# Performance work log

Measured on AMD Instinct MI355X. Metric: run time of the kernel, lower is better.

Reference implementation:

```python
import jax, jax.numpy as jnp
import numpy as np

NUM_HEADS = 128
QK_NOPE = 128
QK_ROPE = 64
V_HEAD = 128
Q_HEAD_DIM = 192
SOFTMAX_SCALE = 1.0 / np.sqrt(192.0)


def _rope_interleave(x, cos, sin):
    # x: [b,h,s,d]; reorder interleaved pairs to half-split layout then rotate
    b, h, s, d = x.shape
    x = x.reshape(b, h, s, d // 2, 2).swapaxes(3, 4).reshape(b, h, s, d)
    x1, x2 = x[..., : d // 2], x[..., d // 2:]
    rot = jnp.concatenate([-x2, x1], axis=-1)
    return x * cos + rot * sin


def setup_inputs() -> dict:
    key = jax.random.key(0)
    ks = jax.random.split(key, 8)
    bsz, q_len = 16, 1
    q_lora, kv_lora = 1536, 512
    cache_cap = 4096
    start_pos = 2048
    s = 0.05
    q_normed_dn = jax.random.normal(ks[0], (bsz, q_len, q_lora), jnp.float32) * s
    compressed_kv = jax.random.normal(ks[1], (bsz, q_len, kv_lora), jnp.float32) * s
    k_pe = jax.random.normal(ks[2], (bsz, 1, q_len, QK_ROPE), jnp.float32) * s
    position_ids = jnp.full((bsz, q_len), start_pos, dtype=jnp.int64)
    ckv_cache = jax.random.normal(ks[3], (bsz, cache_cap, kv_lora), jnp.float32) * s
    k_pe_cache = jax.random.normal(ks[4], (bsz, cache_cap, QK_ROPE), jnp.float32) * s
    # rope caches over full positions
    pos = jnp.arange(cache_cap, dtype=jnp.float32)
    inv = 1.0 / (10000.0 ** (jnp.arange(0, QK_ROPE, 2, dtype=jnp.float32) / QK_ROPE))
    freqs = pos[:, None] * inv[None, :]
    emb = jnp.concatenate([freqs, freqs], axis=-1)
    sin_cache = jnp.sin(emb)
    cos_cache = jnp.cos(emb)
    wkv_b = jax.random.normal(ks[5], (NUM_HEADS, QK_NOPE + V_HEAD, kv_lora), jnp.float32) * s
    wq_b = jax.random.normal(ks[6], (NUM_HEADS * Q_HEAD_DIM, q_lora), jnp.float32) * s
    return {
        "q_normed_dn": q_normed_dn,
        "compressed_kv": compressed_kv,
        "k_pe": k_pe,
        "position_ids": position_ids,
        "start_pos": start_pos,
        "ckv_cache": ckv_cache,
        "k_pe_cache": k_pe_cache,
        "sin_cache": sin_cache,
        "cos_cache": cos_cache,
        "wkv_b": wkv_b,
        "wq_b": wq_b,
    }


def reference(q_normed_dn, compressed_kv, k_pe, position_ids, start_pos,
              ckv_cache, k_pe_cache, sin_cache, cos_cache, wkv_b, wq_b):
    bsz, q_len, q_lora = q_normed_dn.shape
    kv_lora = compressed_kv.shape[-1]

    # split absorbed query projection
    wq_b_t = wq_b.T.reshape(q_lora, NUM_HEADS, Q_HEAD_DIM)  # [l,h,192]
    q_nope = jnp.einsum('bsl,lhd->bhsd', q_normed_dn, wq_b_t[:, :, :QK_NOPE])
    q_pe = jnp.einsum('bsl,lhd->bhsd', q_normed_dn, wq_b_t[:, :, QK_NOPE:])

    # matrix absorption: q_nope projected into latent space via w_ukv
    w_ukv = wkv_b[:, :QK_NOPE]                         # [h,128,c]
    q_nope = jnp.einsum('bshd,hdc->bshc', q_nope.swapaxes(1, 2), w_ukv)  # [b,s,h,c]

    # RoPE on q_pe and k_pe using gathered cos/sin at position_ids
    cos = cos_cache[position_ids][:, None]   # [b,1,s,d]
    sin = sin_cache[position_ids][:, None]
    q_pe = _rope_interleave(q_pe, cos, sin)            # [b,h,s,64]
    k_pe = _rope_interleave(k_pe, cos, sin)            # [b,1,s,64]
    q_pe = q_pe.swapaxes(1, 2)                         # [b,s,h,64]
    k_pe = k_pe[:, 0]                                  # [b,s,64]

    # append new tokens to caches at start_pos (q_len new tokens)
    ckv_cache = jax.lax.dynamic_update_slice(ckv_cache, compressed_kv, (0, start_pos, 0))
    k_pe_cache = jax.lax.dynamic_update_slice(k_pe_cache, k_pe, (0, start_pos, 0))
    kv_len = start_pos + q_len
    ckv = ckv_cache[:, :kv_len]                        # [b,n,c]
    kpe = k_pe_cache[:, :kv_len]                       # [b,n,64]

    # MLA decode attention in latent space (q_len==1, causal trivially satisfied)
    # scores = q_nope . ckv + q_pe . kpe
    scores = (jnp.einsum('bshc,bnc->bhsn', q_nope, ckv) +
              jnp.einsum('bshd,bnd->bhsn', q_pe, kpe)) * SOFTMAX_SCALE
    probs = jax.nn.softmax(scores, axis=-1)
    o = jnp.einsum('bhsn,bnc->bshc', probs, ckv)       # [b,s,h,c]
    o = o.reshape(bsz * q_len, NUM_HEADS, kv_lora)

    # project latent output to v_head_dim via tail of wkv_b
    attn_output = jnp.einsum('bhc,hdc->bhd', o, wkv_b[:, -V_HEAD:])
    return attn_output
```

## Files before the change

kernel.cpp:

```cpp
#include <hip/hip_runtime.h>
#include <hip/hip_bf16.h>
#include <math.h>

typedef __attribute__((ext_vector_type(8))) short short8x;
typedef __attribute__((ext_vector_type(4))) float f32x4;
typedef __attribute__((ext_vector_type(4))) unsigned short u16x4;
typedef __attribute__((ext_vector_type(8))) unsigned short u16x8;

#define NSPLIT 16
#define NTILE 66
#define KVROWS (NTILE * 32)

__device__ __forceinline__ unsigned short f2bf(float x) {
  unsigned int u = __float_as_uint(x);
  u += 0x7fffu + ((u >> 16) & 1u);
  return (unsigned short)(u >> 16);
}
__device__ __forceinline__ float bf2f(unsigned short u) {
  return __uint_as_float(((unsigned int)u) << 16);
}
__device__ __forceinline__ u16x4 cvt4(float4 v) {
  u16x4 r;
  r[0] = f2bf(v.x); r[1] = f2bf(v.y); r[2] = f2bf(v.z); r[3] = f2bf(v.w);
  return r;
}
__device__ __forceinline__ void gload_lds16(const void* g, void* l) {
  __builtin_amdgcn_global_load_lds(
      (const __attribute__((address_space(1))) unsigned int*)g,
      (__attribute__((address_space(3))) unsigned int*)l, 16, 0, 0);
}

__global__ __launch_bounds__(256, 4) void kA(
    const float* __restrict__ ckvc, const float* __restrict__ kpec,
    const float* __restrict__ ckvn, const float* __restrict__ kpein,
    const float* __restrict__ cosc, const float* __restrict__ sinc,
    const int* __restrict__ sposp, int cap,
    unsigned short* __restrict__ kvbf,
    const float* __restrict__ wq, const float* __restrict__ x,
    float* __restrict__ qpart) {
  const int bx = blockIdx.x;
  const int tid = threadIdx.x;

  if (bx < 1536) {
    const int rowblock = bx >> 2, kq = bx & 3;
    const int lane = tid & 63, wid = tid >> 6;
    const int l15 = lane & 15, lg = lane >> 4;
    const int rowb = rowblock * 64 + wid * 16;
    const float* wrow = wq + (size_t)(rowb + l15) * 1536 + kq * 384 + lg * 8;
    const float* xrow = x + (size_t)l15 * 1536 + kq * 384 + lg * 8;

    f32x4 aHH = (f32x4){0.f, 0.f, 0.f, 0.f};
    f32x4 aHL = (f32x4){0.f, 0.f, 0.f, 0.f};
    f32x4 aLH = (f32x4){0.f, 0.f, 0.f, 0.f};
    f32x4 bHH = (f32x4){0.f, 0.f, 0.f, 0.f};
    f32x4 bHL = (f32x4){0.f, 0.f, 0.f, 0.f};
    f32x4 bLH = (f32x4){0.f, 0.f, 0.f, 0.f};

    float4 wA[2], wB[2], xA[2], xB[2];
#pragma unroll
    for (int i = 0; i < 2; ++i) {
      wA[i] = *(const float4*)(wrow + i * 32);
      wB[i] = *(const float4*)(wrow + i * 32 + 4);
      xA[i] = *(const float4*)(xrow + i * 32);
      xB[i] = *(const float4*)(xrow + i * 32 + 4);
    }

#pragma unroll
    for (int kc = 0; kc < 12; ++kc) {
      const int s = kc & 1;
      const float wf[8] = {wA[s].x, wA[s].y, wA[s].z, wA[s].w,
                           wB[s].x, wB[s].y, wB[s].z, wB[s].w};
      const float xf[8] = {xA[s].x, xA[s].y, xA[s].z, xA[s].w,
                           xB[s].x, xB[s].y, xB[s].z, xB[s].w};
      short8x ah, al, bh, bl;
#pragma unroll
      for (int e = 0; e < 8; ++e) {
        const unsigned int wu = __float_as_uint(wf[e]);
        const float whf = __uint_as_float(wu & 0xffff0000u);
        ah[e] = (short)(wu >> 16);
        al[e] = (short)(__float_as_uint(wf[e] - whf) >> 16);
        const unsigned int xu = __float_as_uint(xf[e]);
        const float xhf = __uint_as_float(xu & 0xffff0000u);
        bh[e] = (short)(xu >> 16);
        bl[e] = (short)(__float_as_uint(xf[e] - xhf) >> 16);
      }
      if (kc + 2 < 12) {
        wA[s] = *(const float4*)(wrow + (kc + 2) * 32);
        wB[s] = *(const float4*)(wrow + (kc + 2) * 32 + 4);
        xA[s] = *(const float4*)(xrow + (kc + 2) * 32);
        xB[s] = *(const float4*)(xrow + (kc + 2) * 32 + 4);
      }
      if (kc & 1) {
        bHH = __builtin_amdgcn_mfma_f32_16x16x32_bf16(ah, bh, bHH, 0, 0, 0);
        bHL = __builtin_amdgcn_mfma_f32_16x16x32_bf16(ah, bl, bHL, 0, 0, 0);
        bLH = __builtin_amdgcn_mfma_f32_16x16x32_bf16(al, bh, bLH, 0, 0, 0);
      } else {
        aHH = __builtin_amdgcn_mfma_f32_16x16x32_bf16(ah, bh, aHH, 0, 0, 0);
        aHL = __builtin_amdgcn_mfma_f32_16x16x32_bf16(ah, bl, aHL, 0, 0, 0);
        aLH = __builtin_amdgcn_mfma_f32_16x16x32_bf16(al, bh, aLH, 0, 0, 0);
      }
    }
    const f32x4 acc = (aHH + bHH) + (aHL + bHL) + (aLH + bLH);
#pragma unroll
    for (int r = 0; r < 4; ++r)
      qpart[(size_t)kq * 393216 + (size_t)l15 * 24576 + rowb + lg * 4 + r] = acc[r];
  } else {
    const int bxx = bx - 1536;
    const int spos = sposp[0];
    float4 va[4], vb[4];
    int nn[4], cc[4], bg[4];
#pragma unroll
    for (int g = 0; g < 4; ++g) {
      const int u = bxx * 1024 + g * 256 + tid;
      const int b = u / 152064;
      const int r = u - b * 152064;
      const int n = r / 72;
      const int c8 = (r - n * 72) * 8;
      bg[g] = b; nn[g] = n; cc[g] = c8;
      const float* s0;
      if (n < spos) {
        s0 = (c8 < 512) ? ckvc + ((size_t)b * cap + n) * 512 + c8
                        : kpec + ((size_t)b * cap + n) * 64 + (c8 - 512);
      } else if (n == spos && c8 < 512) {
        s0 = ckvn + (size_t)b * 512 + c8;
      } else {
        s0 = ckvc;
      }
      va[g] = *(const float4*)s0;
      vb[g] = *(const float4*)(s0 + 4);
    }
#pragma unroll
    for (int g = 0; g < 4; ++g) {
      const int u = bxx * 1024 + g * 256 + tid;
      const int n = nn[g], c8 = cc[g], b = bg[g];
      u16x8 w;
      if (n > spos) {
#pragma unroll
        for (int k = 0; k < 8; ++k) w[k] = 0;
      } else if (n == spos && c8 >= 512) {
        const int d = c8 - 512;
        const float* kp = kpein + b * 64;
#pragma unroll
        for (int k = 0; k < 8; ++k) {
          const int dd = d + k;
          const int j = (dd < 32) ? dd : dd - 32;
          const float cj = cosc[spos * 64 + j], sj = sinc[spos * 64 + j];
          const float val = (dd < 32) ? kp[2 * j] * cj - kp[2 * j + 1] * sj
                                      : kp[2 * j + 1] * cj + kp[2 * j] * sj;
          w[k] = f2bf(val);
        }
      } else {
        const u16x4 lo = cvt4(va[g]), hi = cvt4(vb[g]);
#pragma unroll
        for (int k = 0; k < 4; ++k) { w[k] = lo[k]; w[4 + k] = hi[k]; }
      }
      *(u16x8*)(kvbf + (size_t)u * 8) = w;
    }
  }
}

__global__ __launch_bounds__(256) void kB2(
    const float* __restrict__ qpart, const float* __restrict__ wkv,
    const float* __restrict__ cosc, const float* __restrict__ sinc,
    const int* __restrict__ sposp, unsigned short* __restrict__ qcat,
    const unsigned short* __restrict__ kvbf, unsigned short* __restrict__ vT) {
  __shared__ __align__(16) unsigned char shbuf[36864];
  const int bx = blockIdx.x;
  const int tid = threadIdx.x;

  if (bx < 256) {
    float* qs = (float*)shbuf;
    const int h = bx & 127;
    const int half = bx >> 7;
    for (int u = tid; u < 2048; u += 256) {
      int bb = u >> 7, d = u & 127;
      const size_t off = (size_t)bb * 24576 + h * 192 + d;
      qs[u] = qpart[off] + qpart[off + 393216] +
              qpart[off + 786432] + qpart[off + 1179648];
    }
    __syncthreads();
    const int c = half * 256 + tid;
    float acc[16];
#pragma unroll
    for (int bb = 0; bb < 16; ++bb) acc[bb] = 0.f;
    const float* wbase = wkv + (size_t)h * 256 * 512;
    for (int d = 0; d < 128; ++d) {
      const float w = wbase[d * 512 + c];
#pragma unroll
      for (int bb = 0; bb < 16; ++bb) acc[bb] += qs[bb * 128 + d] * w;
    }
#pragma unroll
    for (int bb = 0; bb < 16; ++bb)
      qcat[(size_t)(bb * 128 + h) * 576 + c] = f2bf(acc[bb]);
  } else if (bx < 272) {
    const int b = bx - 256;
    const int pos = sposp[0];
#pragma unroll
    for (int i = 0; i < 16; ++i) {
      int idx = tid + i * 256;
      int h = idx >> 5, j = idx & 31;
      const float cj = cosc[pos * 64 + j];
      const float sj = sinc[pos * 64 + j];
      const size_t base = (size_t)b * 24576 + h * 192 + 128;
      float x0 = qpart[base + 2 * j] + qpart[base + 2 * j + 393216] +
                 qpart[base + 2 * j + 786432] + qpart[base + 2 * j + 1179648];
      float x1 = qpart[base + 2 * j + 1] + qpart[base + 2 * j + 1 + 393216] +
                 qpart[base + 2 * j + 1 + 786432] + qpart[base + 2 * j + 1 + 1179648];
      unsigned short* dst = qcat + (size_t)(b * 128 + h) * 576 + 512;
      dst[j] = f2bf(x0 * cj - x1 * sj);
      dst[j + 32] = f2bf(x1 * cj + x0 * sj);
    }
  } else {
    unsigned short* tile_sh = (unsigned short*)shbuf;
    const int v_ = bx - 272;
    const int b = v_ / NTILE;
    const int tile = v_ - b * NTILE;
    const int wid = tid >> 6;
    const unsigned short* src = kvbf + ((size_t)b * KVROWS + tile * 32) * 576;
#pragma unroll
    for (int i = 0; i < 9; ++i) {
      const int ch = i * 256 + tid;
      const int row = ch / 72, cc = ch - row * 72;
      gload_lds16(src + row * 576 + ((cc ^ (row & 7)) * 8),
                  &tile_sh[(i * 256 + wid * 64) * 8]);
    }
    __syncthreads();
    unsigned short* vdst = vT + ((size_t)b * NTILE + tile) * 18432;
#pragma unroll
    for (int r = 0; r < 9; ++r) {
      const int c = r * 64 + (tid >> 2);
      const int q = tid & 3;
      const int c8 = c >> 3, c7 = c & 7;
      u16x8 w;
#pragma unroll
      for (int j = 0; j < 8; ++j)
        w[j] = tile_sh[(q * 8 + j) * 576 + ((c8 ^ j) << 3) + c7];
      *(u16x8*)(vdst + c * 32 + q * 8) = w;
    }
  }
}

__global__ __launch_bounds__(512, 2) void k4_attn(
    const unsigned short* __restrict__ kvbf, const unsigned short* __restrict__ vT,
    const unsigned short* __restrict__ qcat, const int* __restrict__ sposp,
    unsigned short* __restrict__ opart, float* __restrict__ mlp) {
  __shared__ __align__(16) unsigned short kv_sh[2][32 * 576];
  __shared__ __align__(16) unsigned short vt_sh[2][512 * 32];
  __shared__ __align__(16) unsigned short p_sh[8 * 640];

  const int tid = threadIdx.x;
  const int split = blockIdx.x, b = blockIdx.y;
  const int kvlen = sposp[0] + 1;
  const int lane = tid & 63, wid = tid >> 6;
  const int l15 = lane & 15, lg = lane >> 4;

  const unsigned short* kvb = kvbf + (size_t)b * KVROWS * 576;
  const unsigned short* vtb = vT + (size_t)b * NTILE * 18432;

  const int vro = lane >> 2, vq = lane & 3;
  const int vgq = vq ^ ((vro >> 1) & 3);

  auto STAGE = [&](int pb, int tt) {
    const unsigned short* ksrc = kvb + (size_t)tt * 32 * 576;
    for (int j = wid; j < 36; j += 8) {
      int u = j * 64 + lane;
      int row = u / 72, cc = u - row * 72;
      gload_lds16(ksrc + row * 576 + ((cc ^ (row & 7)) * 8), &kv_sh[pb][j * 512]);
    }
    const unsigned short* vsrc = vtb + (size_t)tt * 18432;
    for (int j = wid; j < 32; j += 8)
      gload_lds16(vsrc + j * 512 + vro * 32 + vgq * 8, &vt_sh[pb][j * 512]);
  };

  STAGE(0, split);

  const int hrow = b * 128 + wid * 16 + l15;
  const unsigned short* qrow = qcat + (size_t)hrow * 576;
  short8x qf[18];
#pragma unroll
  for (int s = 0; s < 18; ++s)
    qf[s] = *(const short8x*)(qrow + s * 32 + lg * 8);

  f32x4 acc[32];
#pragma unroll
  for (int i = 0; i < 32; ++i) acc[i] = (f32x4){0.f, 0.f, 0.f, 0.f};
  float mold[4] = {-1e30f, -1e30f, -1e30f, -1e30f};
  float lsum[4] = {0.f, 0.f, 0.f, 0.f};
  const float C2 = (1.0f / sqrtf(192.0f)) * 1.4426950408889634f;

  const int vrd = ((lg ^ ((l15 >> 1) & 3)) << 3);

  int pb = 0;
  for (int tt = split; tt * 32 < kvlen; tt += NSPLIT, pb ^= 1) {
    __syncthreads();
    if ((tt + NSPLIT) * 32 < kvlen) STAGE(pb ^ 1, tt + NSPLIT);
    const int n0 = tt * 32;

    f32x4 D0 = (f32x4){0.f, 0.f, 0.f, 0.f};
    f32x4 D1 = (f32x4){0.f, 0.f, 0.f, 0.f};
#pragma unroll
    for (int s = 0; s < 18; ++s) {
      const int c8 = (s * 4 + lg) ^ (l15 & 7);
      short8x fb0 = *(const short8x*)&kv_sh[pb][l15 * 576 + c8 * 8];
      short8x fb1 = *(const short8x*)&kv_sh[pb][(16 + l15) * 576 + c8 * 8];
      D0 = __builtin_amdgcn_mfma_f32_16x16x32_bf16(qf[s], fb0, D0, 0, 0, 0);
      D1 = __builtin_amdgcn_mfma_f32_16x16x32_bf16(qf[s], fb1, D1, 0, 0, 0);
    }

    const bool v0 = (n0 + l15) < kvlen;
    const bool v1 = (n0 + 16 + l15) < kvlen;
    float alpha[4];
#pragma unroll
    for (int r = 0; r < 4; ++r) {
      const float t0 = v0 ? D0[r] * C2 : -1e30f;
      const float t1 = v1 ? D1[r] * C2 : -1e30f;
      float mx = fmaxf(t0, t1);
      mx = fmaxf(mx, __shfl_xor(mx, 1, 64));
      mx = fmaxf(mx, __shfl_xor(mx, 2, 64));
      mx = fmaxf(mx, __shfl_xor(mx, 4, 64));
      mx = fmaxf(mx, __shfl_xor(mx, 8, 64));
      const float mn = fmaxf(mold[r], mx);
      alpha[r] = exp2f(mold[r] - mn);
      const float p0 = v0 ? exp2f(t0 - mn) : 0.f;
      const float p1 = v1 ? exp2f(t1 - mn) : 0.f;
      float rs = p0 + p1;
      rs += __shfl_xor(rs, 1, 64);
      rs += __shfl_xor(rs, 2, 64);
      rs += __shfl_xor(rs, 4, 64);
      rs += __shfl_xor(rs, 8, 64);
      lsum[r] = lsum[r] * alpha[r] + rs;
      mold[r] = mn;
      p_sh[wid * 640 + (lg * 4 + r) * 40 + l15] = f2bf(p0);
      p_sh[wid * 640 + (lg * 4 + r) * 40 + 16 + l15] = f2bf(p1);
    }
    const f32x4 av = {alpha[0], alpha[1], alpha[2], alpha[3]};
#pragma unroll
    for (int cg = 0; cg < 32; ++cg) acc[cg] *= av;

    const short8x pa = *(const short8x*)&p_sh[wid * 640 + l15 * 40 + lg * 8];
#pragma unroll
    for (int cg = 0; cg < 32; ++cg) {
      short8x bv = *(const short8x*)&vt_sh[pb][cg * 512 + l15 * 32 + vrd];
      acc[cg] = __builtin_amdgcn_mfma_f32_16x16x32_bf16(pa, bv, acc[cg], 0, 0, 0);
    }
  }

  const int hbm_ = b * 128 + wid * 16 + lg * 4;
  if (l15 == 0) {
#pragma unroll
    for (int r = 0; r < 4; ++r) {
      mlp[(size_t)(hbm_ + r) * (2 * NSPLIT) + split * 2] = mold[r];
      mlp[(size_t)(hbm_ + r) * (2 * NSPLIT) + split * 2 + 1] = lsum[r];
    }
  }

  __syncthreads();
  unsigned short* ep = &kv_sh[0][0] + wid * 8192;
#pragma unroll
  for (int cg = 0; cg < 32; ++cg)
#pragma unroll
    for (int r = 0; r < 4; ++r)
      ep[(lg * 4 + r) * 512 + cg * 16 + l15] = f2bf(acc[cg][r]);
#pragma unroll
  for (int r16 = 0; r16 < 16; ++r16) {
    const int bh = b * 128 + wid * 16 + r16;
    const size_t ob = ((size_t)bh * NSPLIT + split) * 512;
#pragma unroll
    for (int i = 0; i < 2; ++i)
      *(u16x4*)&opart[ob + i * 256 + lane * 4] =
          *(const u16x4*)&ep[r16 * 512 + i * 256 + lane * 4];
  }
}

__global__ __launch_bounds__(512) void kC_out(
    const unsigned short* __restrict__ opart, const float* __restrict__ mlp,
    const float* __restrict__ wkv, float* __restrict__ out) {
  __shared__ float os[16 * 512];
  __shared__ float wsc[16 * 16];
  __shared__ float lsc[16];
  const int h = blockIdx.x;
  const int tid = threadIdx.x;

  if (tid < 16) {
    const int b = tid;
    const float* m = mlp + (size_t)(b * 128 + h) * (2 * NSPLIT);
    float mi[NSPLIT], li[NSPLIT], M = -1e30f;
#pragma unroll
    for (int i = 0; i < NSPLIT; ++i) {
      mi[i] = m[i * 2];
      li[i] = m[i * 2 + 1];
      M = fmaxf(M, mi[i]);
    }
    float Ls = 0.f;
#pragma unroll
    for (int i = 0; i < NSPLIT; ++i) {
      const float w = exp2f(mi[i] - M);
      Ls += li[i] * w;
      wsc[b * NSPLIT + i] = w;
    }
    lsc[b] = Ls;
  }
  __syncthreads();

  for (int u = tid; u < 8192; u += 512) {
    const int b = u >> 9, c = u & 511;
    const unsigned short* op = opart + (size_t)(b * 128 + h) * NSPLIT * 512 + c;
    float o = 0.f;
#pragma unroll
    for (int i = 0; i < NSPLIT; ++i) o += wsc[b * NSPLIT + i] * bf2f(op[i * 512]);
    os[u] = o / lsc[b];
  }
  __syncthreads();

  const int d = tid >> 2, cq = tid & 3;
  const float* wrow = wkv + ((size_t)(h * 256 + 128 + d)) * 512;
  float acc[16];
#pragma unroll
  for (int bb = 0; bb < 16; ++bb) acc[bb] = 0.f;
  for (int i = 0; i < 32; ++i) {
    const int c = cq * 4 + i * 16;
    const float4 w4 = *(const float4*)&wrow[c];
#pragma unroll
    for (int bb = 0; bb < 16; ++bb) {
      const float4 o4 = *(const float4*)&os[bb * 512 + c];
      acc[bb] += w4.x * o4.x + w4.y * o4.y + w4.z * o4.z + w4.w * o4.w;
    }
  }
#pragma unroll
  for (int bb = 0; bb < 16; ++bb) {
    float v = acc[bb];
    v += __shfl_xor(v, 1, 64);
    v += __shfl_xor(v, 2, 64);
    if (cq == 0) out[(size_t)(bb * 128 + h) * 128 + d] = v;
  }
}

extern "C" void kernel_launch(void* const* d_in, const int* in_sizes, int n_in,
                              void* d_out, int out_size, void* d_ws, size_t ws_size,
                              hipStream_t stream) {
  const float* x = (const float*)d_in[0];
  const float* ckvn = (const float*)d_in[1];
  const float* kpein = (const float*)d_in[2];
  const int* sposp = (const int*)d_in[4];
  const float* ckvc = (const float*)d_in[5];
  const float* kpec = (const float*)d_in[6];
  const float* sinc = (const float*)d_in[7];
  const float* cosc = (const float*)d_in[8];
  const float* wkv = (const float*)d_in[9];
  const float* wq = (const float*)d_in[10];
  float* out = (float*)d_out;

  const int cap = in_sizes[5] / (16 * 512);

  float* ws = (float*)d_ws;
  float* qpart = ws;
  float* mlp = ws + 1572864;
  unsigned short* qcat = (unsigned short*)(ws + 1638400);
  unsigned short* kvbf = (unsigned short*)(ws + 2228224);
  unsigned short* vT   = (unsigned short*)(ws + 11960320);
  unsigned short* opart = (unsigned short*)(ws + 21692416);

  kA<<<dim3(1536 + 2376), 256, 0, stream>>>(ckvc, kpec, ckvn, kpein, cosc, sinc,
                                            sposp, cap, kvbf, wq, x, qpart);
  kB2<<<dim3(272 + NTILE * 16), 256, 0, stream>>>(qpart, wkv, cosc, sinc, sposp,
                                                  qcat, kvbf, vT);
  k4_attn<<<dim3(NSPLIT, 16), 512, 0, stream>>>(kvbf, vT, qcat, sposp, opart, mlp);
  kC_out<<<dim3(128), 512, 0, stream>>>(opart, mlp, wkv, out);
}
```

Baseline: 164.3 us.

## Stage KV cache conversion through LDS with async global-to-LDS loads per tile

The fp32-to-bf16 KV cache conversion path in kA now gives each block a 16-row tile of one batch. Full tiles below the current position are staged into shared memory with global_load_lds 16-byte loads, then converted and written. Boundary tiles fall back to a per-element path that handles the new token, the rope rotation and zero padding. The goal is to replace per-thread divides and scattered dual float4 loads with coalesced direct-to-LDS transfers. The cost is 36KB of static LDS per block, which also applies to the GEMM blocks sharing this kernel and may reduce their occupancy.

```diff
diff --git a/kernel.cpp b/kernel.cpp
--- a/kernel.cpp
+++ b/kernel.cpp
@@ -38,6 +38,7 @@
     unsigned short* __restrict__ kvbf,
     const float* __restrict__ wq, const float* __restrict__ x,
     float* __restrict__ qpart) {
+  __shared__ __align__(16) float lf[9216];
   const int bx = blockIdx.x;
   const int tid = threadIdx.x;
 
@@ -106,55 +107,73 @@
       qpart[(size_t)kq * 393216 + (size_t)l15 * 24576 + rowb + lg * 4 + r] = acc[r];
   } else {
     const int bxx = bx - 1536;
+    const int b = bxx / 132;
+    const int tile = bxx - b * 132;
+    const int n0 = tile * 16;
     const int spos = sposp[0];
-    float4 va[4], vb[4];
-    int nn[4], cc[4], bg[4];
-#pragma unroll
-    for (int g = 0; g < 4; ++g) {
-      const int u = bxx * 1024 + g * 256 + tid;
-      const int b = u / 152064;
-      const int r = u - b * 152064;
-      const int n = r / 72;
-      const int c8 = (r - n * 72) * 8;
-      bg[g] = b; nn[g] = n; cc[g] = c8;
-      const float* s0;
-      if (n < spos) {
-        s0 = (c8 < 512) ? ckvc + ((size_t)b * cap + n) * 512 + c8
-                        : kpec + ((size_t)b * cap + n) * 64 + (c8 - 512);
-      } else if (n == spos && c8 < 512) {
-        s0 = ckvn + (size_t)b * 512 + c8;
-      } else {
-        s0 = ckvc;
-      }
-      va[g] = *(const float4*)s0;
-      vb[g] = *(const float4*)(s0 + 4);
-    }
-#pragma unroll
-    for (int g = 0; g < 4; ++g) {
-      const int u = bxx * 1024 + g * 256 + tid;
-      const int n = nn[g], c8 = cc[g], b = bg[g];
-      u16x8 w;
-      if (n > spos) {
-#pragma unroll
-        for (int k = 0; k < 8; ++k) w[k] = 0;
-      } else if (n == spos && c8 >= 512) {
-        const int d = c8 - 512;
-        const float* kp = kpein + b * 64;
-#pragma unroll
-        for (int k = 0; k < 8; ++k) {
-          const int dd = d + k;
-          const int j = (dd < 32) ? dd : dd - 32;
-          const float cj = cosc[spos * 64 + j], sj = sinc[spos * 64 + j];
-          const float val = (dd < 32) ? kp[2 * j] * cj - kp[2 * j + 1] * sj
-                                      : kp[2 * j + 1] * cj + kp[2 * j] * sj;
-          w[k] = f2bf(val);
+    unsigned short* dst = kvbf + ((size_t)b * KVROWS + n0) * 576;
+
+    if (n0 + 15 < spos) {
+      const float* cbase = ckvc + ((size_t)b * cap + n0) * 512;
+      const float* pbase = kpec + ((size_t)b * cap + n0) * 64;
+#pragma unroll
+      for (int i = 0; i < 9; ++i) {
+        const int ch = i * 256 + tid;
+        const int row = ch / 144, cc = ch - row * 144;
+        const float* s = (cc < 128) ? cbase + (size_t)row * 512 + cc * 4
+                                    : pbase + (size_t)row * 64 + (cc - 128) * 4;
+        gload_lds16(s, &lf[(i * 256 + (tid >> 6) * 64) * 4]);
+      }
+      __syncthreads();
+#pragma unroll
+      for (int g = 0; g < 5; ++g) {
+        const int u = g * 256 + tid;
+        if (u < 1152) {
+          const float4 a = *(const float4*)&lf[u * 8];
+          const float4 c2 = *(const float4*)&lf[u * 8 + 4];
+          const u16x4 lo = cvt4(a), hi = cvt4(c2);
+          u16x8 w;
+#pragma unroll
+          for (int k = 0; k < 4; ++k) { w[k] = lo[k]; w[4 + k] = hi[k]; }
+          *(u16x8*)(dst + (size_t)u * 8) = w;
         }
-      } else {
-        const u16x4 lo = cvt4(va[g]), hi = cvt4(vb[g]);
-#pragma unroll
-        for (int k = 0; k < 4; ++k) { w[k] = lo[k]; w[4 + k] = hi[k]; }
-      }
-      *(u16x8*)(kvbf + (size_t)u * 8) = w;
+      }
+    } else {
+#pragma unroll
+      for (int g = 0; g < 5; ++g) {
+        const int u = g * 256 + tid;
+        if (u < 1152) {
+          const int row = u / 72, c8 = (u - row * 72) * 8;
+          const int n = n0 + row;
+          u16x8 w;
+          if (n > spos) {
+#pragma unroll
+            for (int k = 0; k < 8; ++k) w[k] = 0;
+          } else if (n == spos && c8 >= 512) {
+            const int d = c8 - 512;
+            const float* kp = kpein + b * 64;
+#pragma unroll
+            for (int k = 0; k < 8; ++k) {
+              const int dd = d + k;
+              const int j = (dd < 32) ? dd : dd - 32;
+              const float cj = cosc[spos * 64 + j], sj = sinc[spos * 64 + j];
+              const float val = (dd < 32) ? kp[2 * j] * cj - kp[2 * j + 1] * sj
+                                          : kp[2 * j + 1] * cj + kp[2 * j] * sj;
+              w[k] = f2bf(val);
+            }
+          } else {
+            const float* s0;
+            if (n == spos) s0 = ckvn + (size_t)b * 512 + c8;
+            else s0 = (c8 < 512) ? ckvc + ((size_t)b * cap + n) * 512 + c8
+                                 : kpec + ((size_t)b * cap + n) * 64 + (c8 - 512);
+            const u16x4 lo = cvt4(*(const float4*)s0);
+            const u16x4 hi = cvt4(*(const float4*)(s0 + 4));
+#pragma unroll
+            for (int k = 0; k < 4; ++k) { w[k] = lo[k]; w[4 + k] = hi[k]; }
+          }
+          *(u16x8*)(dst + (size_t)u * 8) = w;
+        }
+      }
     }
   }
 }
@@ -460,7 +479,7 @@
   unsigned short* vT   = (unsigned short*)(ws + 11960320);
   unsigned short* opart = (unsigned short*)(ws + 21692416);
 
-  kA<<<dim3(1536 + 2376), 256, 0, stream>>>(ckvc, kpec, ckvn, kpein, cosc, sinc,
+  kA<<<dim3(1536 + 2112), 256, 0, stream>>>(ckvc, kpec, ckvn, kpein, cosc, sinc,
                                             sposp, cap, kvbf, wq, x, qpart);
   kB2<<<dim3(272 + NTILE * 16), 256, 0, stream>>>(qpart, wkv, cosc, sinc, sposp,
                                                   qcat, kvbf, vT);
```

After: 163.2 us, median of 2. Within noise of the previous version (-0.6%).
